# Kernel optimization log

Measured on AMD Instinct MI355X. Metric: run time of the kernel, lower is better.

The kernel has to match this reference:

```python
import jax, jax.numpy as jnp
import numpy as np
from jax import lax

K = 3          # kernel size
PAD = 1        # 'same' padding for k=3: (1,1,1,1)
STRIDE = 1
DIL = 1
OFFSET_SIZE = 2 * K * K  # deformable_groups=1


def setup_inputs() -> dict:
    key = jax.random.key(0)
    k1, k2, k3, k4 = jax.random.split(key, 4)
    B, H, W, C = 8, 64, 64, 256
    F = 256
    inputs = jax.random.normal(k1, (B, H, W, C), dtype=jnp.float32)
    # offset/mask branch conv: small weights so sampled offsets are modest
    om_kernel = jax.random.normal(k2, (K, K, C, OFFSET_SIZE * 3 // 2), dtype=jnp.float32) * 0.01
    om_bias = jnp.zeros((OFFSET_SIZE * 3 // 2,), dtype=jnp.float32)
    stdv = 1.0 / np.sqrt(K * K * C)
    kernel = jax.random.uniform(k3, (K * K * C, F), dtype=jnp.float32, minval=-stdv, maxval=stdv)
    bias = jax.random.normal(k4, (1, 1, 1, F), dtype=jnp.float32) * 0.01
    return {"inputs": inputs, "om_kernel": om_kernel, "om_bias": om_bias,
            "kernel": kernel, "bias": bias}


def _dcnv2(x, om_kernel, om_bias, kernel, bias):
    B, H, W, C = x.shape
    # offset/mask branch (same conv geometry as the deformable conv)
    om = lax.conv_general_dilated(
        x, om_kernel, window_strides=(STRIDE, STRIDE),
        padding=((PAD, PAD), (PAD, PAD)), rhs_dilation=(DIL, DIL),
        dimension_numbers=('NHWC', 'HWIO', 'NHWC')) + om_bias
    OH, OW = om.shape[1], om.shape[2]
    KK = K * K
    offset = om[..., :OFFSET_SIZE].reshape(B, OH, OW, KK, 2)  # (dy, dx) per kernel point
    mask = jax.nn.sigmoid(om[..., OFFSET_SIZE:]) * 2.0         # [B,OH,OW,KK]

    # base sampling grid per output pixel and kernel point
    kk = jnp.arange(KK)
    ky = (kk // K).astype(jnp.float32)
    kx = (kk % K).astype(jnp.float32)
    base_y = jnp.arange(OH, dtype=jnp.float32)[:, None] * STRIDE - PAD + ky[None, :] * DIL  # [OH,KK]
    base_x = jnp.arange(OW, dtype=jnp.float32)[:, None] * STRIDE - PAD + kx[None, :] * DIL  # [OW,KK]

    py = base_y[None, :, None, :] + offset[..., 0]  # [B,OH,OW,KK]
    px = base_x[None, None, :, :] + offset[..., 1]

    y0 = jnp.floor(py); x0 = jnp.floor(px)
    wy1 = py - y0; wy0 = 1.0 - wy1
    wx1 = px - x0; wx0 = 1.0 - wx1

    bi = jnp.arange(B)[:, None, None, None]

    def gather(yi, xi):
        # zero-padded bilinear corner fetch
        valid = (yi >= 0) & (yi <= H - 1) & (xi >= 0) & (xi <= W - 1)
        yc = jnp.clip(yi, 0, H - 1).astype(jnp.int32)
        xc = jnp.clip(xi, 0, W - 1).astype(jnp.int32)
        v = x[bi, yc, xc]  # [B,OH,OW,KK,C]
        return v * valid[..., None].astype(x.dtype)

    y1 = y0 + 1.0; x1 = x0 + 1.0
    cols = (gather(y0, x0) * (wy0 * wx0)[..., None]
            + gather(y0, x1) * (wy0 * wx1)[..., None]
            + gather(y1, x0) * (wy1 * wx0)[..., None]
            + gather(y1, x1) * (wy1 * wx1)[..., None])
    cols = cols * mask[..., None]  # modulation, [B,OH,OW,KK,C]

    out = cols.reshape(B, OH, OW, KK * C) @ kernel  # [B,OH,OW,F]
    return out + bias


def reference(inputs, om_kernel, om_bias, kernel, bias):
    return _dcnv2(inputs, om_kernel, om_bias, kernel, bias)
```

## Files before the change

### kernel.cpp

```cpp
#include <hip/hip_runtime.h>
#include <math.h>


#define BB 8
#define HH 64
#define WW 64
#define CIN 256
#define FF 256
#define KPTS 9
#define OCH 27
#define MT 64
#define NS2 36

typedef _Float16 half8  __attribute__((ext_vector_type(8)));
typedef _Float16 half4v __attribute__((ext_vector_type(4)));
typedef float    floatx4 __attribute__((ext_vector_type(4)));

__device__ __forceinline__ int aoff(int m, int g) {
    return m * 64 + ((g ^ (m & 7)) << 3);
}

__device__ __forceinline__ half8 splat8(_Float16 v) {
    half8 r = {v, v, v, v, v, v, v, v};
    return r;
}

#define XBLK 4096
__global__ __launch_bounds__(256) void convert_all(
    const float* __restrict__ x, const float* __restrict__ wmat,
    const float* __restrict__ omw,
    _Float16* __restrict__ xh, _Float16* __restrict__ wsB, _Float16* __restrict__ wsOM)
{
    const int bid = blockIdx.x;
    if (bid < XBLK) {
        if (xh == nullptr) return;
        const size_t i = ((size_t)bid * 256 + threadIdx.x) * 8;
        const floatx4 a = *(const floatx4*)(x + i);
        const floatx4 b = *(const floatx4*)(x + i + 4);
        half8 h;
        h[0] = (_Float16)a.x; h[1] = (_Float16)a.y; h[2] = (_Float16)a.z; h[3] = (_Float16)a.w;
        h[4] = (_Float16)b.x; h[5] = (_Float16)b.y; h[6] = (_Float16)b.z; h[7] = (_Float16)b.w;
        *(half8*)(xh + i) = h;
    } else if (bid < XBLK + 288) {
        const int kg = bid - XBLK;
        const int n  = threadIdx.x;
        half8 h;
        #pragma unroll
        for (int j = 0; j < 8; ++j)
            h[j] = (_Float16)wmat[(size_t)(kg * 8 + j) * FF + n];
        ((half8*)wsB)[(size_t)kg * FF + n] = h;
    } else {
        const int t = (bid - XBLK - 288) * 256 + threadIdx.x;
        const int k = t >> 5, n = t & 31;
        const float v = (n < OCH) ? omw[k * OCH + n] : 0.f;
        wsOM[((size_t)(k >> 3) * 32 + n) * 8 + (k & 7)] = (_Float16)v;
    }
}

template <bool F16X>
__global__ __launch_bounds__(512, 4) void dcn_mfma4(
    const float* __restrict__ x,
    const _Float16* __restrict__ xh,
    const float* __restrict__ omb,
    const _Float16* __restrict__ wsB,
    const _Float16* __restrict__ wsOM,
    const float* __restrict__ bias,
    float* __restrict__ out)
{
    __shared__ _Float16 Ah0[MT * 64];
    __shared__ _Float16 Ah1[MT * 64];
    __shared__ float    om_s[MT][28];
    __shared__ half4v   cwS[MT][KPTS];
    __shared__ int4     caS[MT][KPTS];

    const int tid  = threadIdx.x;
    const int w    = tid >> 6;
    const int lane = tid & 63;
    const int q    = lane >> 4;
    const int lr   = lane & 15;
    const int ms   = tid >> 3;
    const int qc   = tid & 7;

    const int p  = blockIdx.x;
    const int b  = p & 7;
    const int oh = p >> 3;
    const int pbase = (b * HH + oh) * WW;

    const half8* wsOM8 = (const half8*)wsOM;
    const half8* wsB8  = (const half8*)wsB;

    const int mt1 = w & 3;
    const int nt1 = w >> 2;
    floatx4 acc1 = {0.f, 0.f, 0.f, 0.f};

    auto load1 = [&](int sp) -> half8 {
        sp = sp < NS2 - 1 ? sp : NS2 - 1;
        const int kk = sp >> 2, cb = (sp & 3) << 6;
        const int ky = kk / 3, kx = kk - ky * 3;
        const int iy = oh - 1 + ky, ix = ms - 1 + kx;
        half8 v = {(_Float16)0, (_Float16)0, (_Float16)0, (_Float16)0,
                   (_Float16)0, (_Float16)0, (_Float16)0, (_Float16)0};
        if (iy >= 0 && iy < HH && ix >= 0 && ix < WW) {
            const int idx = ((b * HH + iy) * WW + ix) * CIN + cb + qc * 8;
            if constexpr (F16X) {
                v = *(const half8*)(xh + idx);
            } else {
                const floatx4 lo = *(const floatx4*)(x + idx);
                const floatx4 hi = *(const floatx4*)(x + idx + 4);
                v[0] = (_Float16)lo.x; v[1] = (_Float16)lo.y;
                v[2] = (_Float16)lo.z; v[3] = (_Float16)lo.w;
                v[4] = (_Float16)hi.x; v[5] = (_Float16)hi.y;
                v[6] = (_Float16)hi.z; v[7] = (_Float16)hi.w;
            }
        }
        return v;
    };
    auto loadB1 = [&](int sp, half8& b0, half8& b1) {
        sp = sp < NS2 - 1 ? sp : NS2 - 1;
        b0 = wsOM8[(sp * 8 + q) * 32 + nt1 * 16 + lr];
        b1 = wsOM8[(sp * 8 + 4 + q) * 32 + nt1 * 16 + lr];
    };

    half8 vp;
    half8 bo00, bo01, bo10, bo11;
    {
        const half8 v0 = load1(0);
        *(half8*)(Ah0 + aoff(ms, qc)) = v0;
        vp = load1(1);
        loadB1(0, bo00, bo01);
    }
    for (int s = 0; s < NS2; s += 2) {
        __syncthreads();
        *(half8*)(Ah1 + aoff(ms, qc)) = vp;
        vp = load1(s + 2);
        loadB1(s + 1, bo10, bo11);
        {
            const half8 a0 = *(const half8*)(Ah0 + aoff(mt1 * 16 + lr, q));
            const half8 a1 = *(const half8*)(Ah0 + aoff(mt1 * 16 + lr, 4 + q));
            acc1 = __builtin_amdgcn_mfma_f32_16x16x32_f16(a0, bo00, acc1, 0, 0, 0);
            acc1 = __builtin_amdgcn_mfma_f32_16x16x32_f16(a1, bo01, acc1, 0, 0, 0);
        }
        __syncthreads();
        *(half8*)(Ah0 + aoff(ms, qc)) = vp;
        vp = load1(s + 3);
        loadB1(s + 2, bo00, bo01);
        {
            const half8 a0 = *(const half8*)(Ah1 + aoff(mt1 * 16 + lr, q));
            const half8 a1 = *(const half8*)(Ah1 + aoff(mt1 * 16 + lr, 4 + q));
            acc1 = __builtin_amdgcn_mfma_f32_16x16x32_f16(a0, bo10, acc1, 0, 0, 0);
            acc1 = __builtin_amdgcn_mfma_f32_16x16x32_f16(a1, bo11, acc1, 0, 0, 0);
        }
    }
    {
        const int och = nt1 * 16 + lr;
        if (och < OCH) {
            const float ob = omb[och];
            #pragma unroll
            for (int reg = 0; reg < 4; ++reg) {
                const int m = mt1 * 16 + q * 4 + reg;
                om_s[m][och] = acc1[reg] + ob;
            }
        }
    }
    __syncthreads();

    for (int i = tid; i < MT * KPTS; i += 512) {
        const int m = i / KPTS, kk = i % KPTS;
        const int ky = kk / 3, kx = kk - ky * 3;
        const float dy = om_s[m][2 * kk];
        const float dx = om_s[m][2 * kk + 1];
        const float mask = 2.f / (1.f + __expf(-om_s[m][18 + kk]));
        const float py = (float)(oh - 1 + ky) + dy;
        const float px = (float)(m - 1 + kx) + dx;
        const float y0f = floorf(py), x0f = floorf(px);
        const float wy1 = py - y0f, wx1 = px - x0f;
        const float wy0 = 1.f - wy1, wx0 = 1.f - wx1;
        const int y0 = (int)y0f, x0 = (int)x0f;
        const int y1 = y0 + 1, x1 = x0 + 1;
        const bool vy0 = (y0 >= 0) && (y0 < HH);
        const bool vy1 = (y1 >= 0) && (y1 < HH);
        const bool vx0 = (x0 >= 0) && (x0 < WW);
        const bool vx1 = (x1 >= 0) && (x1 < WW);
        const int y0c = min(max(y0, 0), HH - 1), y1c = min(max(y1, 0), HH - 1);
        const int x0c = min(max(x0, 0), WW - 1), x1c = min(max(x1, 0), WW - 1);
        const int rb = b * HH;
        int4 ca;
        ca.x = ((rb + y0c) * WW + x0c) * CIN;
        ca.y = ((rb + y0c) * WW + x1c) * CIN;
        ca.z = ((rb + y1c) * WW + x0c) * CIN;
        ca.w = ((rb + y1c) * WW + x1c) * CIN;
        half4v cw;
        cw.x = (_Float16)((vy0 && vx0) ? mask * wy0 * wx0 : 0.f);
        cw.y = (_Float16)((vy0 && vx1) ? mask * wy0 * wx1 : 0.f);
        cw.z = (_Float16)((vy1 && vx0) ? mask * wy1 * wx0 : 0.f);
        cw.w = (_Float16)((vy1 && vx1) ? mask * wy1 * wx1 : 0.f);
        caS[m][kk] = ca;
        cwS[m][kk] = cw;
    }
    __syncthreads();

    floatx4 acc[2][4];
    #pragma unroll
    for (int t = 0; t < 2; ++t)
        #pragma unroll
        for (int nt = 0; nt < 4; ++nt)
            acc[t][nt] = (floatx4){0.f, 0.f, 0.f, 0.f};

    const int mh  = w & 1;
    const int nh  = w >> 1;
    const int n0w = nh * 64;

    half8   pc0, pc1, pc2, pc3;
    floatx4 fa0, fb0, fa1, fb1, fa2, fb2, fa3, fb3;
    half4v  pcw;

    auto pre2 = [&](int sp) {
        sp = sp < NS2 - 1 ? sp : NS2 - 1;
        const int c  = (sp * 456) >> 12;
        const int kk = sp - c * 9;
        const int co = c * 64 + qc * 8;
        const int4 ca = caS[ms][kk];
        pcw = cwS[ms][kk];
        if constexpr (F16X) {
            pc0 = *(const half8*)(xh + ca.x + co);
            pc1 = *(const half8*)(xh + ca.y + co);
            pc2 = *(const half8*)(xh + ca.z + co);
            pc3 = *(const half8*)(xh + ca.w + co);
        } else {
            fa0 = *(const floatx4*)(x + ca.x + co); fb0 = *(const floatx4*)(x + ca.x + co + 4);
            fa1 = *(const floatx4*)(x + ca.y + co); fb1 = *(const floatx4*)(x + ca.y + co + 4);
            fa2 = *(const floatx4*)(x + ca.z + co); fb2 = *(const floatx4*)(x + ca.z + co + 4);
            fa3 = *(const floatx4*)(x + ca.w + co); fb3 = *(const floatx4*)(x + ca.w + co + 4);
        }
    };
    auto comb = [&]() -> half8 {
        if constexpr (F16X) {
            const half8 w0 = splat8(pcw.x), w1 = splat8(pcw.y);
            const half8 w2 = splat8(pcw.z), w3 = splat8(pcw.w);
            return pc0 * w0 + pc1 * w1 + pc2 * w2 + pc3 * w3;
        } else {
            const float w0 = (float)pcw.x, w1 = (float)pcw.y;
            const float w2 = (float)pcw.z, w3 = (float)pcw.w;
            const floatx4 lo = w0 * fa0 + w1 * fa1 + w2 * fa2 + w3 * fa3;
            const floatx4 hi = w0 * fb0 + w1 * fb1 + w2 * fb2 + w3 * fb3;
            half8 r;
            r[0] = (_Float16)lo.x; r[1] = (_Float16)lo.y;
            r[2] = (_Float16)lo.z; r[3] = (_Float16)lo.w;
            r[4] = (_Float16)hi.x; r[5] = (_Float16)hi.y;
            r[6] = (_Float16)hi.z; r[7] = (_Float16)hi.w;
            return r;
        }
    };

    half8 bP[2][4];
    auto loadB2 = [&](int sp) {
        const int c  = (sp * 456) >> 12;
        const int kk = sp - c * 9;
        const int r8 = kk * 32 + c * 8;
        #pragma unroll
        for (int kh = 0; kh < 2; ++kh)
            #pragma unroll
            for (int nt = 0; nt < 4; ++nt)
                bP[kh][nt] = wsB8[(size_t)(r8 + kh * 4 + q) * FF + n0w + nt * 16 + lr];
    };

    {
        pre2(0);
        const half8 v0 = comb();
        *(half8*)(Ah0 + aoff(ms, qc)) = v0;
        pre2(1);
    }
    for (int s = 0; s < NS2; s += 2) {
        __syncthreads();
        {
            const half8 v = comb();
            *(half8*)(Ah1 + aoff(ms, qc)) = v;
        }
        loadB2(s);
        pre2(s + 2);
        #pragma unroll
        for (int kh = 0; kh < 2; ++kh) {
            half8 afr[2];
            #pragma unroll
            for (int t = 0; t < 2; ++t)
                afr[t] = *(const half8*)(Ah0 + aoff((mh * 2 + t) * 16 + lr, kh * 4 + q));
            #pragma unroll
            for (int nt = 0; nt < 4; ++nt)
                #pragma unroll
                for (int t = 0; t < 2; ++t)
                    acc[t][nt] = __builtin_amdgcn_mfma_f32_16x16x32_f16(afr[t], bP[kh][nt], acc[t][nt], 0, 0, 0);
        }
        __syncthreads();
        {
            const half8 v = comb();
            *(half8*)(Ah0 + aoff(ms, qc)) = v;
        }
        loadB2(s + 1);
        pre2(s + 3);
        #pragma unroll
        for (int kh = 0; kh < 2; ++kh) {
            half8 afr[2];
            #pragma unroll
            for (int t = 0; t < 2; ++t)
                afr[t] = *(const half8*)(Ah1 + aoff((mh * 2 + t) * 16 + lr, kh * 4 + q));
            #pragma unroll
            for (int nt = 0; nt < 4; ++nt)
                #pragma unroll
                for (int t = 0; t < 2; ++t)
                    acc[t][nt] = __builtin_amdgcn_mfma_f32_16x16x32_f16(afr[t], bP[kh][nt], acc[t][nt], 0, 0, 0);
        }
    }

    #pragma unroll
    for (int nt = 0; nt < 4; ++nt) {
        const int f = n0w + nt * 16 + lr;
        const float bv = bias[f];
        #pragma unroll
        for (int t = 0; t < 2; ++t)
            #pragma unroll
            for (int reg = 0; reg < 4; ++reg) {
                const int m = (mh * 2 + t) * 16 + q * 4 + reg;
                out[(size_t)(pbase + m) * FF + f] = acc[t][nt][reg] + bv;
            }
    }
}

#define MTILE 32
#define CHUNK 64
#define NCHUNK (CIN / CHUNK)

__global__ __launch_bounds__(256) void dcn_fused(
    const float* __restrict__ x, const float* __restrict__ omw,
    const float* __restrict__ omb, const float* __restrict__ wmat,
    const float* __restrict__ bias, float* __restrict__ out)
{
    __shared__ float A[CHUNK][MTILE + 1];
    __shared__ float om_s[MTILE][28];
    __shared__ float cw[MTILE][4];
    __shared__ int   ca[MTILE][4];

    const int tid = threadIdx.x;
    const int pbase = blockIdx.x * MTILE;
    const int ccid = tid & 63;
    const int mg2 = tid >> 6;
    const int och = tid & 31;
    const int mg1 = tid >> 5;
    float acc1[4] = {0.f, 0.f, 0.f, 0.f};

    for (int kk = 0; kk < KPTS; ++kk) {
        const int ky = kk / 3, kx = kk % 3;
        for (int ch = 0; ch < NCHUNK; ++ch) {
            const int cbase = ch * CHUNK;
            __syncthreads();
            #pragma unroll
            for (int i = 0; i < 8; ++i) {
                const int m = mg2 * 8 + i;
                const int pp = pbase + m;
                const int bb = pp >> 12, oh = (pp >> 6) & 63, ow = pp & 63;
                const int iy = oh - 1 + ky, ix = ow - 1 + kx;
                float v = 0.f;
                if (iy >= 0 && iy < HH && ix >= 0 && ix < WW)
                    v = x[((bb * HH + iy) * WW + ix) * CIN + cbase + ccid];
                A[ccid][m] = v;
            }
            __syncthreads();
            if (och < OCH) {
                for (int cc = 0; cc < CHUNK; ++cc) {
                    const float bv = omw[((kk * CIN) + cbase + cc) * OCH + och];
                    #pragma unroll
                    for (int i = 0; i < 4; ++i)
                        acc1[i] += A[cc][mg1 * 4 + i] * bv;
                }
            }
        }
    }
    __syncthreads();
    if (och < OCH) {
        const float ob = omb[och];
        #pragma unroll
        for (int i = 0; i < 4; ++i)
            om_s[mg1 * 4 + i][och] = acc1[i] + ob;
    }
    __syncthreads();

    const int f4 = (tid & 63) * 4;
    const int mgc = tid >> 6;
    float acc[8][4];
    #pragma unroll
    for (int j = 0; j < 8; ++j)
        #pragma unroll
        for (int i = 0; i < 4; ++i) acc[j][i] = 0.f;

    for (int kk = 0; kk < KPTS; ++kk) {
        if (tid < MTILE) {
            const int m = tid;
            const int pp = pbase + m;
            const int bb = pp >> 12, oh = (pp >> 6) & 63, ow = pp & 63;
            const int ky = kk / 3, kx = kk % 3;
            const float dy = om_s[m][2 * kk];
            const float dx = om_s[m][2 * kk + 1];
            const float mask = 2.f / (1.f + __expf(-om_s[m][18 + kk]));
            const float py = (float)(oh - 1 + ky) + dy;
            const float px = (float)(ow - 1 + kx) + dx;
            const float y0f = floorf(py), x0f = floorf(px);
            const float wy1 = py - y0f, wx1 = px - x0f;
            const float wy0 = 1.f - wy1, wx0 = 1.f - wx1;
            const int y0 = (int)y0f, x0 = (int)x0f;
            const int y1 = y0 + 1, x1 = x0 + 1;
            const bool vy0 = (y0 >= 0) && (y0 < HH);
            const bool vy1 = (y1 >= 0) && (y1 < HH);
            const bool vx0 = (x0 >= 0) && (x0 < WW);
            const bool vx1 = (x1 >= 0) && (x1 < WW);
            const int y0c = min(max(y0, 0), HH - 1), y1c = min(max(y1, 0), HH - 1);
            const int x0c = min(max(x0, 0), WW - 1), x1c = min(max(x1, 0), WW - 1);
            const int rb = bb * HH;
            ca[m][0] = ((rb + y0c) * WW + x0c) * CIN;
            ca[m][1] = ((rb + y0c) * WW + x1c) * CIN;
            ca[m][2] = ((rb + y1c) * WW + x0c) * CIN;
            ca[m][3] = ((rb + y1c) * WW + x1c) * CIN;
            cw[m][0] = (vy0 && vx0) ? mask * wy0 * wx0 : 0.f;
            cw[m][1] = (vy0 && vx1) ? mask * wy0 * wx1 : 0.f;
            cw[m][2] = (vy1 && vx0) ? mask * wy1 * wx0 : 0.f;
            cw[m][3] = (vy1 && vx1) ? mask * wy1 * wx1 : 0.f;
        }
        for (int ch = 0; ch < NCHUNK; ++ch) {
            const int cbase = ch * CHUNK;
            __syncthreads();
            #pragma unroll
            for (int i = 0; i < 8; ++i) {
                const int m = mg2 * 8 + i;
                const int cidx = cbase + ccid;
                const float v = cw[m][0] * x[ca[m][0] + cidx]
                              + cw[m][1] * x[ca[m][1] + cidx]
                              + cw[m][2] * x[ca[m][2] + cidx]
                              + cw[m][3] * x[ca[m][3] + cidx];
                A[ccid][m] = v;
            }
            __syncthreads();
            const float* brow = wmat + (size_t)(kk * CIN + cbase) * FF + f4;
            for (int cc = 0; cc < CHUNK; ++cc) {
                const float4 bv = *(const float4*)(brow + cc * FF);
                #pragma unroll
                for (int j = 0; j < 8; ++j) {
                    const float a = A[cc][mgc * 8 + j];
                    acc[j][0] += a * bv.x;
                    acc[j][1] += a * bv.y;
                    acc[j][2] += a * bv.z;
                    acc[j][3] += a * bv.w;
                }
            }
        }
    }

    const float4 bb4 = *(const float4*)(bias + f4);
    #pragma unroll
    for (int j = 0; j < 8; ++j) {
        const int m = mgc * 8 + j;
        const int pp = pbase + m;
        float4 o;
        o.x = acc[j][0] + bb4.x;
        o.y = acc[j][1] + bb4.y;
        o.z = acc[j][2] + bb4.z;
        o.w = acc[j][3] + bb4.w;
        *(float4*)(out + (size_t)pp * FF + f4) = o;
    }
}

extern "C" void kernel_launch(void* const* d_in, const int* in_sizes, int n_in,
                              void* d_out, int out_size, void* d_ws, size_t ws_size,
                              hipStream_t stream) {
    const float* x    = (const float*)d_in[0];
    const float* omw  = (const float*)d_in[1];
    const float* omb  = (const float*)d_in[2];
    const float* wmat = (const float*)d_in[3];
    const float* bias = (const float*)d_in[4];
    float* out = (float*)d_out;

    const size_t needB  = (size_t)2304 * FF * sizeof(_Float16);
    const size_t needOM = (size_t)288 * 32 * 8 * sizeof(_Float16);
    const size_t needX  = (size_t)BB * HH * WW * CIN * sizeof(_Float16);

    if (ws_size >= needB + needOM + needX) {
        _Float16* wsB  = (_Float16*)d_ws;
        _Float16* wsOM = (_Float16*)((char*)d_ws + needB);
        _Float16* xh   = (_Float16*)((char*)d_ws + needB + needOM);
        convert_all<<<XBLK + 288 + 288, 256, 0, stream>>>(x, wmat, omw, xh, wsB, wsOM);
        dcn_mfma4<true><<<BB * HH, 512, 0, stream>>>(x, xh, omb, wsB, wsOM, bias, out);
    } else if (ws_size >= needB + needOM) {
        _Float16* wsB  = (_Float16*)d_ws;
        _Float16* wsOM = (_Float16*)((char*)d_ws + needB);
        convert_all<<<XBLK + 288 + 288, 256, 0, stream>>>(x, wmat, omw, nullptr, wsB, wsOM);
        dcn_mfma4<false><<<BB * HH, 512, 0, stream>>>(x, nullptr, omb, wsB, wsOM, bias, out);
    } else {
        const int nblocks = (BB * HH * WW) / MTILE;
        dcn_fused<<<nblocks, 256, 0, stream>>>(x, omw, omb, wmat, bias, out);
    }
}
```

Measured before the change: 166.9 us.

## Halve row tile to 32 pixels with 256-thread blocks, reorder K loop kk-major

Result: faster. 163.4 us (-2.1%).

```diff
diff --git a/kernel.cpp b/kernel.cpp
--- a/kernel.cpp
+++ b/kernel.cpp
@@ -9,7 +9,7 @@
 #define FF 256
 #define KPTS 9
 #define OCH 27
-#define MT 64
+#define MT 32
 #define NS2 36
 
 typedef _Float16 half8  __attribute__((ext_vector_type(8)));
@@ -58,7 +58,7 @@
 }
 
 template <bool F16X>
-__global__ __launch_bounds__(512, 4) void dcn_mfma4(
+__global__ __launch_bounds__(256, 4) void dcn_mfma5(
     const float* __restrict__ x,
     const _Float16* __restrict__ xh,
     const float* __restrict__ omb,
@@ -81,23 +81,25 @@
     const int ms   = tid >> 3;
     const int qc   = tid & 7;
 
-    const int p  = blockIdx.x;
-    const int b  = p & 7;
-    const int oh = p >> 3;
-    const int pbase = (b * HH + oh) * WW;
+    const int p   = blockIdx.x;
+    const int b   = p & 7;
+    const int r   = p >> 3;
+    const int oh  = r >> 1;
+    const int owb = (r & 1) * MT;
+    const int pbase = (b * HH + oh) * WW + owb;
 
     const half8* wsOM8 = (const half8*)wsOM;
     const half8* wsB8  = (const half8*)wsB;
 
-    const int mt1 = w & 3;
-    const int nt1 = w >> 2;
+    const int mt1 = w & 1;
+    const int nt1 = w >> 1;
     floatx4 acc1 = {0.f, 0.f, 0.f, 0.f};
 
     auto load1 = [&](int sp) -> half8 {
         sp = sp < NS2 - 1 ? sp : NS2 - 1;
         const int kk = sp >> 2, cb = (sp & 3) << 6;
         const int ky = kk / 3, kx = kk - ky * 3;
-        const int iy = oh - 1 + ky, ix = ms - 1 + kx;
+        const int iy = oh - 1 + ky, ix = owb + ms - 1 + kx;
         half8 v = {(_Float16)0, (_Float16)0, (_Float16)0, (_Float16)0,
                    (_Float16)0, (_Float16)0, (_Float16)0, (_Float16)0};
         if (iy >= 0 && iy < HH && ix >= 0 && ix < WW) {
@@ -164,14 +166,14 @@
     }
     __syncthreads();
 
-    for (int i = tid; i < MT * KPTS; i += 512) {
+    for (int i = tid; i < MT * KPTS; i += 256) {
         const int m = i / KPTS, kk = i % KPTS;
         const int ky = kk / 3, kx = kk - ky * 3;
         const float dy = om_s[m][2 * kk];
         const float dx = om_s[m][2 * kk + 1];
         const float mask = 2.f / (1.f + __expf(-om_s[m][18 + kk]));
         const float py = (float)(oh - 1 + ky) + dy;
-        const float px = (float)(m - 1 + kx) + dx;
+        const float px = (float)(owb + m - 1 + kx) + dx;
         const float y0f = floorf(py), x0f = floorf(px);
         const float wy1 = py - y0f, wx1 = px - x0f;
         const float wy0 = 1.f - wy1, wx0 = 1.f - wx1;
@@ -206,9 +208,7 @@
         for (int nt = 0; nt < 4; ++nt)
             acc[t][nt] = (floatx4){0.f, 0.f, 0.f, 0.f};
 
-    const int mh  = w & 1;
-    const int nh  = w >> 1;
-    const int n0w = nh * 64;
+    const int n0w = w * 64;
 
     half8   pc0, pc1, pc2, pc3;
     floatx4 fa0, fb0, fa1, fb1, fa2, fb2, fa3, fb3;
@@ -216,9 +216,8 @@
 
     auto pre2 = [&](int sp) {
         sp = sp < NS2 - 1 ? sp : NS2 - 1;
-        const int c  = (sp * 456) >> 12;
-        const int kk = sp - c * 9;
-        const int co = c * 64 + qc * 8;
+        const int kk = sp >> 2;
+        const int co = ((sp & 3) << 6) + qc * 8;
         const int4 ca = caS[ms][kk];
         pcw = cwS[ms][kk];
         if constexpr (F16X) {
@@ -254,9 +253,8 @@
 
     half8 bP[2][4];
     auto loadB2 = [&](int sp) {
-        const int c  = (sp * 456) >> 12;
-        const int kk = sp - c * 9;
-        const int r8 = kk * 32 + c * 8;
+        const int kk = sp >> 2;
+        const int r8 = kk * 32 + (sp & 3) * 8;
         #pragma unroll
         for (int kh = 0; kh < 2; ++kh)
             #pragma unroll
@@ -283,7 +281,7 @@
             half8 afr[2];
             #pragma unroll
             for (int t = 0; t < 2; ++t)
-                afr[t] = *(const half8*)(Ah0 + aoff((mh * 2 + t) * 16 + lr, kh * 4 + q));
+                afr[t] = *(const half8*)(Ah0 + aoff(t * 16 + lr, kh * 4 + q));
             #pragma unroll
             for (int nt = 0; nt < 4; ++nt)
                 #pragma unroll
@@ -302,7 +300,7 @@
             half8 afr[2];
             #pragma unroll
             for (int t = 0; t < 2; ++t)
-                afr[t] = *(const half8*)(Ah1 + aoff((mh * 2 + t) * 16 + lr, kh * 4 + q));
+                afr[t] = *(const half8*)(Ah1 + aoff(t * 16 + lr, kh * 4 + q));
             #pragma unroll
             for (int nt = 0; nt < 4; ++nt)
                 #pragma unroll
@@ -319,7 +317,7 @@
         for (int t = 0; t < 2; ++t)
             #pragma unroll
             for (int reg = 0; reg < 4; ++reg) {
-                const int m = (mh * 2 + t) * 16 + q * 4 + reg;
+                const int m = t * 16 + q * 4 + reg;
                 out[(size_t)(pbase + m) * FF + f] = acc[t][nt][reg] + bv;
             }
     }
@@ -485,12 +483,12 @@
         _Float16* wsOM = (_Float16*)((char*)d_ws + needB);
         _Float16* xh   = (_Float16*)((char*)d_ws + needB + needOM);
         convert_all<<<XBLK + 288 + 288, 256, 0, stream>>>(x, wmat, omw, xh, wsB, wsOM);
-        dcn_mfma4<true><<<BB * HH, 512, 0, stream>>>(x, xh, omb, wsB, wsOM, bias, out);
+        dcn_mfma5<true><<<BB * HH * 2, 256, 0, stream>>>(x, xh, omb, wsB, wsOM, bias, out);
     } else if (ws_size >= needB + needOM) {
         _Float16* wsB  = (_Float16*)d_ws;
         _Float16* wsOM = (_Float16*)((char*)d_ws + needB);
         convert_all<<<XBLK + 288 + 288, 256, 0, stream>>>(x, wmat, omw, nullptr, wsB, wsOM);
-        dcn_mfma4<false><<<BB * HH, 512, 0, stream>>>(x, nullptr, omb, wsB, wsOM, bias, out);
+        dcn_mfma5<false><<<BB * HH * 2, 256, 0, stream>>>(x, nullptr, omb, wsB, wsOM, bias, out);
     } else {
         const int nblocks = (BB * HH * WW) / MTILE;
         dcn_fused<<<nblocks, 256, 0, stream>>>(x, omw, omb, wmat, bias, out);
```
